# Kernel optimization log

Measured on AMD Instinct MI355X. Metric: run time of the kernel, lower is better.

## Reference

```python
import jax, jax.numpy as jnp
import numpy as np

B, C, L, H, D = 2, 1024, 2048, 16, 64  # batch, n_factor, seq, heads, head_dim
LN_EPS = 1e-5


def setup_inputs() -> dict:
    key = jax.random.key(0)
    ks = jax.random.split(key, 8)
    s = 0.02
    return {
        "x": jax.random.normal(ks[0], (B, C, L), jnp.float32),
        "y": jax.random.normal(ks[1], (B, C, L), jnp.float32),
        "Wq": jax.random.normal(ks[2], (H, C, D), jnp.float32) * s,
        "Wk": jax.random.normal(ks[3], (H, C, D), jnp.float32) * s,
        "Wv": jax.random.normal(ks[4], (H, C, D), jnp.float32) * s,
        "bq": jax.random.normal(ks[5], (H, D), jnp.float32) * s,
        "bk": jax.random.normal(ks[6], (H, D), jnp.float32) * s,
        "bv": jax.random.normal(ks[7], (H, D), jnp.float32) * s,
        "gamma": jnp.ones((C,), jnp.float32),
        "beta": jnp.zeros((C,), jnp.float32),
    }


def reference(x, y, Wq, Wk, Wv, bq, bk, bv, gamma, beta):
    # Per-head Conv1d(kernel=1) == per-position linear; batch all heads at once.
    # x,y: [B, C, L]; W*: [H, C, D]; result q/k/v: [B, H, L, D]
    q = jnp.einsum('bcl,hcd->bhld', x, Wq) + bq[None, :, None, :]
    k = jnp.einsum('bcl,hcd->bhld', y, Wk) + bk[None, :, None, :]
    v = jnp.einsum('bcl,hcd->bhld', y, Wv) + bv[None, :, None, :]

    scale = 1.0 / jnp.sqrt(jnp.float32(D))  # n_factor_head ** 0.5
    scores = jnp.einsum('bhqd,bhkd->bhqk', q, k) * scale  # [B,H,L,L]
    attn = jax.nn.softmax(scores, axis=-1)
    ctx = jnp.einsum('bhqk,bhkd->bhqd', attn, v)  # [B,H,L,D]

    # torch.cat over heads along last dim == [B, L, H*D]
    att = jnp.transpose(ctx, (0, 2, 1, 3)).reshape(B, L, H * D)

    h = jnp.transpose(x, (0, 2, 1)) + att  # residual on x permuted to [B,L,C]
    mu = jnp.mean(h, axis=-1, keepdims=True)
    var = jnp.var(h, axis=-1, keepdims=True)
    out = (h - mu) * jax.lax.rsqrt(var + LN_EPS) * gamma + beta
    # dropout: identity in eval mode
    return out
```

## Files before the change

kernel.cpp:

```cpp
#include <hip/hip_runtime.h>
#include <hip/hip_bf16.h>

#define DEVI __device__ __forceinline__

typedef unsigned short u16;
typedef __bf16 bf16x8 __attribute__((ext_vector_type(8)));
typedef float f32x4 __attribute__((ext_vector_type(4)));

constexpr int Bn = 2, Cn = 1024, Ln = 2048, Hn = 16, Dn = 64;

DEVI u16 f2bfu(float f) { return __builtin_bit_cast(u16, __float2bfloat16(f)); }
DEVI float bfu2f(u16 u) { return __bfloat162float(__builtin_bit_cast(__hip_bfloat16, u)); }
DEVI f32x4 mfma16(bf16x8 a, bf16x8 b, f32x4 c) {
  return __builtin_amdgcn_mfma_f32_16x16x32_bf16(a, b, c, 0, 0, 0);
}
DEVI unsigned pk2(float lo, float hi) {
  return (unsigned)f2bfu(lo) | ((unsigned)f2bfu(hi) << 16);
}
DEVI void gld16(const u16* g, u16* l) {
  __builtin_amdgcn_global_load_lds(
      (const __attribute__((address_space(1))) unsigned*)g,
      (__attribute__((address_space(3))) unsigned*)l, 16, 0, 0);
}
DEVI int fsw(int row) { return (row & 7) ^ (((row >> 3) & 1) << 2); }

__global__ __launch_bounds__(256) void transpose_xy(const float* __restrict__ x,
                                                    const float* __restrict__ y,
                                                    u16* __restrict__ xT,
                                                    u16* __restrict__ yT) {
  int z = blockIdx.z;
  int which = z >> 1, b = z & 1;
  const float* src = (which ? y : x) + (size_t)b * Cn * Ln;
  u16* dst = (which ? yT : xT) + (size_t)b * Ln * Cn;
  int l0 = blockIdx.x * 64, c0 = blockIdx.y * 64;
  __shared__ float tile[64][65];
  int t = threadIdx.x;
  #pragma unroll
  for (int i = 0; i < 16; ++i) {
    int idx = i * 256 + t;
    int r = idx >> 6, cc = idx & 63;
    tile[r][cc] = src[(size_t)(c0 + r) * Ln + (l0 + cc)];
  }
  __syncthreads();
  #pragma unroll
  for (int i = 0; i < 8; ++i) {
    int idx = i * 256 + t;
    int r = idx >> 5, cc = (idx & 31) * 2;
    unsigned pkv = pk2(tile[cc][r], tile[cc + 1][r]);
    *(unsigned*)(&dst[(size_t)(l0 + r) * Cn + (c0 + cc)]) = pkv;
  }
}

__global__ __launch_bounds__(256) void transpose_w(const float* __restrict__ Wq,
                                                   const float* __restrict__ Wk,
                                                   const float* __restrict__ Wv,
                                                   u16* __restrict__ WT) {
  int c0 = blockIdx.x * 64, h = blockIdx.y, which = blockIdx.z;
  const float* src = (which == 0 ? Wq : (which == 1 ? Wk : Wv)) + (size_t)h * Cn * Dn;
  u16* dst = WT + ((size_t)which * Hn + h) * Dn * Cn;
  __shared__ float tile[64][65];
  int t = threadIdx.x;
  #pragma unroll
  for (int i = 0; i < 16; ++i) {
    int idx = i * 256 + t;
    int r = idx >> 6, cc = idx & 63;
    tile[r][cc] = src[(size_t)(c0 + r) * Dn + cc];
  }
  __syncthreads();
  #pragma unroll
  for (int i = 0; i < 16; ++i) {
    int idx = i * 256 + t;
    int r = idx >> 6, cc = idx & 63;
    dst[(size_t)r * Cn + (c0 + cc)] = f2bfu(tile[cc][r]);
  }
}

__global__ __launch_bounds__(256) void gemm_qkv3(const u16* __restrict__ xT,
                                                 const u16* __restrict__ yT,
                                                 const u16* __restrict__ WT,
                                                 const float* __restrict__ bq,
                                                 const float* __restrict__ bk,
                                                 const float* __restrict__ bv,
                                                 u16* __restrict__ Qb,
                                                 u16* __restrict__ Kb,
                                                 u16* __restrict__ Vt) {
  int mt = blockIdx.x, by = blockIdx.y, b = blockIdx.z;
  int which = by >> 3, hp = by & 7;
  const u16* A = (which == 0 ? xT : yT) + (size_t)b * Ln * Cn + (size_t)mt * 128 * Cn;
  const u16* Bw = WT + ((size_t)which * 1024 + (size_t)hp * 128) * Cn;
  __shared__ __align__(16) u16 smem[2 * 128 * 64];
  u16* lA = smem;
  u16* lB = smem + 128 * 64;
  int t = threadIdx.x, wave = t >> 6, lane = t & 63;
  int wr = wave >> 1, wc = wave & 1;
  int ml = lane & 15, kg = lane >> 4;
  f32x4 acc[4][4] = {};
  for (int k0 = 0; k0 < Cn; k0 += 64) {
    __syncthreads();
    #pragma unroll
    for (int j = 0; j < 4; ++j) {
      int q = wave * 256 + j * 64 + lane;
      int row = q >> 3, p = q & 7, c16 = p ^ (row & 7);
      gld16(A + (size_t)row * Cn + k0 + c16 * 8, &lA[(wave * 256 + j * 64) * 8]);
    }
    #pragma unroll
    for (int j = 0; j < 4; ++j) {
      int q = wave * 256 + j * 64 + lane;
      int row = q >> 3, p = q & 7, c16 = p ^ (row & 7);
      gld16(Bw + (size_t)row * Cn + k0 + c16 * 8, &lB[(wave * 256 + j * 64) * 8]);
    }
    __syncthreads();
    bf16x8 af[4][2], bf[4][2];
    #pragma unroll
    for (int m = 0; m < 4; ++m) {
      int row = wr * 64 + m * 16 + ml;
      #pragma unroll
      for (int kk = 0; kk < 2; ++kk) {
        int p = (kk * 4 + kg) ^ (row & 7);
        af[m][kk] = *(const bf16x8*)(&lA[row * 64 + p * 8]);
      }
    }
    #pragma unroll
    for (int n = 0; n < 4; ++n) {
      int row = wc * 64 + n * 16 + ml;
      #pragma unroll
      for (int kk = 0; kk < 2; ++kk) {
        int p = (kk * 4 + kg) ^ (row & 7);
        bf[n][kk] = *(const bf16x8*)(&lB[row * 64 + p * 8]);
      }
    }
    __builtin_amdgcn_s_setprio(1);
    #pragma unroll
    for (int m = 0; m < 4; ++m)
      #pragma unroll
      for (int n = 0; n < 4; ++n)
        #pragma unroll
        for (int kk = 0; kk < 2; ++kk)
          acc[m][n] = mfma16(af[m][kk], bf[n][kk], acc[m][n]);
    __builtin_amdgcn_s_setprio(0);
  }
  int head = hp * 2 + wc;
  const float* bp = (which == 0 ? bq : (which == 1 ? bk : bv));
  if (which < 2) {
    u16* O = (which == 0 ? Qb : Kb) + (((size_t)b * Hn + head) * Ln + (size_t)mt * 128) * Dn;
    #pragma unroll
    for (int n = 0; n < 4; ++n) {
      float bvv = bp[head * 64 + n * 16 + ml];
      #pragma unroll
      for (int m = 0; m < 4; ++m)
        #pragma unroll
        for (int r = 0; r < 4; ++r) {
          int row = wr * 64 + m * 16 + kg * 4 + r;
          O[(size_t)row * Dn + n * 16 + ml] = f2bfu(acc[m][n][r] + bvv);
        }
    }
  } else {
    __syncthreads();
    #pragma unroll
    for (int n = 0; n < 4; ++n) {
      float bvv = bp[head * 64 + n * 16 + ml];
      int n_loc = wc * 64 + n * 16 + ml;
      int swz = (n_loc & 7) << 4;
      #pragma unroll
      for (int m = 0; m < 4; ++m) {
        int m_base = wr * 64 + m * 16 + kg * 4;
        uint2 pkd;
        pkd.x = pk2(acc[m][n][0] + bvv, acc[m][n][1] + bvv);
        pkd.y = pk2(acc[m][n][2] + bvv, acc[m][n][3] + bvv);
        *(uint2*)(&smem[n_loc * 128 + (m_base ^ swz)]) = pkd;
      }
    }
    __syncthreads();
    u16* Vbase = Vt + ((size_t)b * Hn + hp * 2) * Dn * Ln + (size_t)mt * 128;
    #pragma unroll
    for (int i = 0; i < 8; ++i) {
      int chunk = i * 256 + t;
      int n = chunk >> 4, cc = chunk & 15;
      uint4 vv = *(const uint4*)(&smem[n * 128 + (cc ^ ((n & 7) << 1)) * 8]);
      *(uint4*)(Vbase + (size_t)n * Ln + cc * 8) = vv;
    }
  }
}

__global__ __launch_bounds__(512, 8) void flash_attn(const u16* __restrict__ Qg,
                                                     const u16* __restrict__ Kg,
                                                     const u16* __restrict__ Vtg,
                                                     u16* __restrict__ att) {
  int n = blockIdx.x + 32 * (blockIdx.y + 16 * blockIdx.z);
  int xcd = n & 7, m = n >> 3;
  int grp = xcd * 4 + (m >> 5);
  int qt = m & 31;
  int h = grp & 15, b = grp >> 4;

  size_t bh = (size_t)b * Hn + h;
  const u16* Qp = Qg + (bh * Ln + (size_t)qt * 64) * Dn;
  const u16* Kp = Kg + bh * Ln * Dn;
  const u16* Vp = Vtg + bh * Dn * Ln;
  int t = threadIdx.x, wave = t >> 6, lane = t & 63;
  int qs = wave & 3, g = wave >> 2;
  int ml = lane & 15, kg = lane >> 4;
  __shared__ __align__(16) u16 Kl[2][64 * 64];
  __shared__ __align__(16) u16 Vl[2][64 * 64];

  constexpr float QS = 0.125f * 1.44269504f;
  bf16x8 qf[2];
  #pragma unroll
  for (int kk = 0; kk < 2; ++kk) {
    bf16x8 raw = *(const bf16x8*)(Qp + (size_t)(qs * 16 + ml) * Dn + kk * 32 + kg * 8);
    #pragma unroll
    for (int j = 0; j < 8; ++j) raw[j] = (__bf16)((float)raw[j] * QS);
    qf[kk] = raw;
  }

  f32x4 ctx[4] = {};
  float psum = 0.f;

  auto stage = [&](int buf, int kv0) {
    int rowk = t >> 3, p = t & 7, c16 = p ^ fsw(rowk);
    gld16(Kp + (size_t)(kv0 + rowk) * Dn + c16 * 8, &Kl[buf][wave * 512]);
    gld16(Vp + (size_t)rowk * Ln + kv0 + c16 * 8, &Vl[buf][wave * 512]);
  };

  stage(0, 0);
  __syncthreads();

  constexpr int NT = Ln / 64;
  for (int tt = 0; tt < NT; ++tt) {
    int cur = tt & 1;
    if (tt + 1 < NT) stage(cur ^ 1, (tt + 1) * 64);
    const u16* Kh = Kl[cur];
    const u16* Vh = Vl[cur];
    f32x4 s[2] = {};
    __builtin_amdgcn_s_setprio(1);
    #pragma unroll
    for (int nt = 0; nt < 2; ++nt) {
      int rowk = g * 32 + 8 * (ml >> 2) + 4 * nt + (ml & 3);
      #pragma unroll
      for (int kk = 0; kk < 2; ++kk) {
        int p = (kk * 4 + kg) ^ fsw(rowk);
        bf16x8 kf = *(const bf16x8*)(&Kh[rowk * 64 + p * 8]);
        s[nt] = mfma16(kf, qf[kk], s[nt]);
      }
    }
    __builtin_amdgcn_s_setprio(0);
    f32x4 e0, e1;
    #pragma unroll
    for (int r = 0; r < 4; ++r) e0[r] = __builtin_amdgcn_exp2f(s[0][r]);
    #pragma unroll
    for (int r = 0; r < 4; ++r) e1[r] = __builtin_amdgcn_exp2f(s[1][r]);
    psum += (e0[0] + e0[1]) + (e0[2] + e0[3]) + (e1[0] + e1[1]) + (e1[2] + e1[3]);
    uint4 pw;
    pw.x = pk2(e0[0], e0[1]);
    pw.y = pk2(e0[2], e0[3]);
    pw.z = pk2(e1[0], e1[1]);
    pw.w = pk2(e1[2], e1[3]);
    bf16x8 pf = __builtin_bit_cast(bf16x8, pw);
    __builtin_amdgcn_s_setprio(1);
    #pragma unroll
    for (int nt = 0; nt < 4; ++nt) {
      int rowv = nt * 16 + ml;
      int p = (g * 4 + kg) ^ fsw(rowv);
      bf16x8 vf = *(const bf16x8*)(&Vh[rowv * 64 + p * 8]);
      ctx[nt] = mfma16(pf, vf, ctx[nt]);
    }
    __builtin_amdgcn_s_setprio(0);
    if (tt + 1 < NT) __syncthreads();
  }
  __syncthreads();
  float* comb = (float*)&Kl[0][0];
  float* psA = (float*)&Vl[0][0];
  if (g == 1) {
    int base = qs * 1024 + lane;
    #pragma unroll
    for (int nt = 0; nt < 4; ++nt)
      #pragma unroll
      for (int r = 0; r < 4; ++r)
        comb[base + (nt * 4 + r) * 64] = ctx[nt][r];
    psA[qs * 64 + lane] = psum;
  }
  __syncthreads();
  if (g == 0) {
    int base = qs * 1024 + lane;
    #pragma unroll
    for (int nt = 0; nt < 4; ++nt)
      #pragma unroll
      for (int r = 0; r < 4; ++r)
        ctx[nt][r] += comb[base + (nt * 4 + r) * 64];
    psum += psA[qs * 64 + lane];
    psum += __shfl_xor(psum, 16);
    psum += __shfl_xor(psum, 32);
    float inv[4];
    #pragma unroll
    for (int r = 0; r < 4; ++r) inv[r] = 1.f / __shfl(psum, kg * 4 + r);
    #pragma unroll
    for (int nt = 0; nt < 4; ++nt)
      #pragma unroll
      for (int r = 0; r < 4; ++r) {
        size_t row = (size_t)b * Ln + qt * 64 + qs * 16 + kg * 4 + r;
        att[row * Cn + h * Dn + nt * 16 + ml] = f2bfu(ctx[nt][r] * inv[r]);
      }
  }
}

__global__ __launch_bounds__(256) void ln_kernel(const u16* __restrict__ att,
                                                 const u16* __restrict__ xT,
                                                 const float* __restrict__ gamma,
                                                 const float* __restrict__ beta,
                                                 float* __restrict__ out) {
  size_t row = blockIdx.x;
  const u16* ap = att + row * Cn;
  const u16* xp = xT + row * Cn;
  float* op = out + row * Cn;
  int t = threadIdx.x;
  ushort4 a4 = *(const ushort4*)(ap + t * 4);
  ushort4 xv = *(const ushort4*)(xp + t * 4);
  float h0 = bfu2f(a4.x) + bfu2f(xv.x), h1 = bfu2f(a4.y) + bfu2f(xv.y);
  float h2 = bfu2f(a4.z) + bfu2f(xv.z), h3 = bfu2f(a4.w) + bfu2f(xv.w);
  float s = h0 + h1 + h2 + h3;
  float ss = h0 * h0 + h1 * h1 + h2 * h2 + h3 * h3;
  #pragma unroll
  for (int off = 1; off < 64; off <<= 1) {
    s += __shfl_xor(s, off);
    ss += __shfl_xor(ss, off);
  }
  __shared__ float red[8];
  int wave = t >> 6, lane = t & 63;
  if (lane == 0) { red[wave] = s; red[wave + 4] = ss; }
  __syncthreads();
  s = red[0] + red[1] + red[2] + red[3];
  ss = red[4] + red[5] + red[6] + red[7];
  float mu = s * (1.f / 1024.f);
  float var = ss * (1.f / 1024.f) - mu * mu;
  float rinv = rsqrtf(var + 1e-5f);
  float4 gmv = *(const float4*)(gamma + t * 4);
  float4 bev = *(const float4*)(beta + t * 4);
  float4 o;
  o.x = (h0 - mu) * rinv * gmv.x + bev.x;
  o.y = (h1 - mu) * rinv * gmv.y + bev.y;
  o.z = (h2 - mu) * rinv * gmv.z + bev.z;
  o.w = (h3 - mu) * rinv * gmv.w + bev.w;
  *(float4*)(op + t * 4) = o;
}

extern "C" void kernel_launch(void* const* d_in, const int* in_sizes, int n_in,
                              void* d_out, int out_size, void* d_ws, size_t ws_size,
                              hipStream_t stream) {
  const float* x = (const float*)d_in[0];
  const float* y = (const float*)d_in[1];
  const float* Wq = (const float*)d_in[2];
  const float* Wk = (const float*)d_in[3];
  const float* Wv = (const float*)d_in[4];
  const float* bq = (const float*)d_in[5];
  const float* bk = (const float*)d_in[6];
  const float* bv = (const float*)d_in[7];
  const float* gamma = (const float*)d_in[8];
  const float* beta = (const float*)d_in[9];
  float* out = (float*)d_out;

  char* ws = (char*)d_ws;
  u16* xT = (u16*)(ws + 0);
  u16* yT = (u16*)(ws + 8388608);
  u16* WT = (u16*)(ws + 16777216);
  u16* Qb = (u16*)(ws + 23068672);
  u16* Kb = (u16*)(ws + 31457280);
  u16* VT = (u16*)(ws + 39845888);
  u16* att = (u16*)(ws + 48234496);

  transpose_xy<<<dim3(Ln / 64, Cn / 64, 4), dim3(256), 0, stream>>>(x, y, xT, yT);
  transpose_w<<<dim3(Cn / 64, Hn, 3), dim3(256), 0, stream>>>(Wq, Wk, Wv, WT);
  gemm_qkv3<<<dim3(Ln / 128, 24, Bn), dim3(256), 0, stream>>>(xT, yT, WT, bq, bk, bv, Qb, Kb, VT);
  flash_attn<<<dim3(Ln / 64, Hn, Bn), dim3(512), 0, stream>>>(Qb, Kb, VT, att);
  ln_kernel<<<dim3(Bn * Ln), dim3(256), 0, stream>>>(att, xT, gamma, beta, out);
}
```

Measured before the change: 109.8 us.

## Use explicit vmcnt waits and split barriers in attention KV double-buffer loop

Replaces the per-tile __syncthreads with explicit s_waitcnt vmcnt(2) plus s_barrier, so the prefetch of the next K/V tile stays in flight while the current tile is consumed. The loop is unrolled by two so buffer indices are compile-time constants, and swizzled LDS offsets are hoisted out of the loop. The intent is to cut synchronisation stalls and address arithmetic. It depends on exact vmcnt accounting for the direct-to-LDS loads, and a wrong count would create a race.

```diff
diff --git a/kernel.cpp b/kernel.cpp
--- a/kernel.cpp
+++ b/kernel.cpp
@@ -215,33 +215,51 @@
   f32x4 ctx[4] = {};
   float psum = 0.f;
 
+  int koff[2][2], voff[4];
+  {
+    #pragma unroll
+    for (int nt = 0; nt < 2; ++nt) {
+      int rowk = g * 32 + 8 * (ml >> 2) + 4 * nt + (ml & 3);
+      #pragma unroll
+      for (int kk = 0; kk < 2; ++kk)
+        koff[nt][kk] = rowk * 64 + (((kk * 4 + kg) ^ fsw(rowk)) << 3);
+    }
+    #pragma unroll
+    for (int nt = 0; nt < 4; ++nt) {
+      int rowv = nt * 16 + ml;
+      voff[nt] = rowv * 64 + ((((g * 4 + kg) ^ fsw(rowv))) << 3);
+    }
+  }
+  int rowk_st = t >> 3;
+  int c16_st = ((t & 7) ^ fsw(rowk_st)) * 8;
+
   auto stage = [&](int buf, int kv0) {
-    int rowk = t >> 3, p = t & 7, c16 = p ^ fsw(rowk);
-    gld16(Kp + (size_t)(kv0 + rowk) * Dn + c16 * 8, &Kl[buf][wave * 512]);
-    gld16(Vp + (size_t)rowk * Ln + kv0 + c16 * 8, &Vl[buf][wave * 512]);
+    gld16(Kp + (size_t)(kv0 + rowk_st) * Dn + c16_st, &Kl[buf][wave * 512]);
+    gld16(Vp + (size_t)rowk_st * Ln + kv0 + c16_st, &Vl[buf][wave * 512]);
   };
 
-  stage(0, 0);
-  __syncthreads();
-
   constexpr int NT = Ln / 64;
-  for (int tt = 0; tt < NT; ++tt) {
-    int cur = tt & 1;
-    if (tt + 1 < NT) stage(cur ^ 1, (tt + 1) * 64);
+
+  auto tile = [&](int cur, int tt) {
+    if (tt + 1 < NT) {
+      stage(cur ^ 1, (tt + 1) * 64);
+      asm volatile("s_waitcnt vmcnt(2)" ::: "memory");
+    } else {
+      asm volatile("s_waitcnt vmcnt(0)" ::: "memory");
+    }
+    __builtin_amdgcn_s_barrier();
+    __builtin_amdgcn_sched_barrier(0);
     const u16* Kh = Kl[cur];
     const u16* Vh = Vl[cur];
     f32x4 s[2] = {};
     __builtin_amdgcn_s_setprio(1);
     #pragma unroll
-    for (int nt = 0; nt < 2; ++nt) {
-      int rowk = g * 32 + 8 * (ml >> 2) + 4 * nt + (ml & 3);
+    for (int nt = 0; nt < 2; ++nt)
       #pragma unroll
       for (int kk = 0; kk < 2; ++kk) {
-        int p = (kk * 4 + kg) ^ fsw(rowk);
-        bf16x8 kf = *(const bf16x8*)(&Kh[rowk * 64 + p * 8]);
+        bf16x8 kf = *(const bf16x8*)(&Kh[koff[nt][kk]]);
         s[nt] = mfma16(kf, qf[kk], s[nt]);
       }
-    }
     __builtin_amdgcn_s_setprio(0);
     f32x4 e0, e1;
     #pragma unroll
@@ -258,14 +276,23 @@
     __builtin_amdgcn_s_setprio(1);
     #pragma unroll
     for (int nt = 0; nt < 4; ++nt) {
-      int rowv = nt * 16 + ml;
-      int p = (g * 4 + kg) ^ fsw(rowv);
-      bf16x8 vf = *(const bf16x8*)(&Vh[rowv * 64 + p * 8]);
+      bf16x8 vf = *(const bf16x8*)(&Vh[voff[nt]]);
       ctx[nt] = mfma16(pf, vf, ctx[nt]);
     }
     __builtin_amdgcn_s_setprio(0);
-    if (tt + 1 < NT) __syncthreads();
-  }
+    asm volatile("s_waitcnt lgkmcnt(0)" ::: "memory");
+    __builtin_amdgcn_s_barrier();
+  };
+
+  stage(0, 0);
+  asm volatile("s_waitcnt vmcnt(0)" ::: "memory");
+  __builtin_amdgcn_s_barrier();
+
+  for (int tt = 0; tt < NT; tt += 2) {
+    tile(0, tt);
+    tile(1, tt + 1);
+  }
+
   __syncthreads();
   float* comb = (float*)&Kl[0][0];
   float* psA = (float*)&Vl[0][0];
```

New measurement: 108.5 us. Within noise of the previous version (-1.2%).
